# Kernel tuning notes

Measured on AMD Instinct MI355X. Metric: run time of the kernel, lower is better.

Reference implementation:

```python
import jax, jax.numpy as jnp
import numpy as np

N_NODES = 50000
N_EDGES = 800000
IN_SIZE = 128
HIDDEN = 128   # out_size * 2
OUT_SIZE = 64


def setup_inputs() -> dict:
    key = jax.random.key(0)
    ks = jax.random.split(key, 6)
    h = jax.random.normal(ks[0], (N_NODES, IN_SIZE), dtype=jnp.float32)
    W1 = jax.random.normal(ks[1], (IN_SIZE, HIDDEN), dtype=jnp.float32) * (1.0 / np.sqrt(IN_SIZE))
    b1 = jnp.zeros((HIDDEN,), dtype=jnp.float32)
    W2 = jax.random.normal(ks[2], (HIDDEN, OUT_SIZE), dtype=jnp.float32) * (1.0 / np.sqrt(HIDDEN))
    b2 = jnp.zeros((OUT_SIZE,), dtype=jnp.float32)
    src = jax.random.randint(ks[3], (N_EDGES,), 0, N_NODES, dtype=jnp.int64)
    dst = jax.random.randint(ks[4], (N_EDGES,), 0, N_NODES, dtype=jnp.int64)
    return {"h": h, "W1": W1, "b1": b1, "W2": W2, "b2": b2, "src": src, "dst": dst}


def _norms(src, dst, n_nodes):
    # DGL GraphConv norm='both': scale by out_degree^{-1/2} (src side)
    # and in_degree^{-1/2} (dst side); zero degrees clamped to 1.
    ones = jnp.ones(src.shape, dtype=jnp.float32)
    out_deg = jnp.maximum(jax.ops.segment_sum(ones, src, num_segments=n_nodes), 1.0)
    in_deg = jnp.maximum(jax.ops.segment_sum(ones, dst, num_segments=n_nodes), 1.0)
    return (out_deg ** -0.5)[:, None], (in_deg ** -0.5)[:, None]


def _graph_conv(x, W, b, src, dst, norm_out, norm_in, n_nodes):
    # h' = D_in^{-1/2} A D_out^{-1/2} x W + b
    x = x * norm_out                                   # [N, F]
    agg = jax.ops.segment_sum(x[src], dst, num_segments=n_nodes)  # SpMM: [N, F]
    return (agg * norm_in) @ W + b


def reference(h, W1, b1, W2, b2, src, dst):
    n_nodes = h.shape[0]
    norm_out, norm_in = _norms(src, dst, n_nodes)
    h = jax.nn.relu(_graph_conv(h, W1, b1, src, dst, norm_out, norm_in, n_nodes))
    h = jax.nn.relu(_graph_conv(h, W2, b2, src, dst, norm_out, norm_in, n_nodes))
    return h
```

## Files before the change

### kernel.cpp

```cpp
#include <hip/hip_runtime.h>

#define N_NODES 50000
#define N_EDGES 800000
#define CHUNKS 128
#define CHUNK_EDGES 6250
#define NBS 196
#define GA_BLOCKS 391
#define PLACE_BLOCKS 3125

typedef __attribute__((ext_vector_type(8))) short bf16x8;
typedef __attribute__((ext_vector_type(4))) float f32x4;

static __device__ inline unsigned short bf16_rne(float x) {
    unsigned ua = __float_as_uint(x);
    return (unsigned short)((ua + 0x7fffu + ((ua >> 16) & 1u)) >> 16);
}

static __device__ inline unsigned short f16_bits(float x) {
    _Float16 hx = (_Float16)x;
    return __builtin_bit_cast(unsigned short, hx);
}

static __device__ inline float f16_val(unsigned short u) {
    return (float)__builtin_bit_cast(_Float16, u);
}

static __device__ inline float2 unpack_f16x2(unsigned u) {
    _Float16 lo = __builtin_bit_cast(_Float16, (unsigned short)(u & 0xffffu));
    _Float16 hi = __builtin_bit_cast(_Float16, (unsigned short)(u >> 16));
    return make_float2((float)lo, (float)hi);
}

__global__ __launch_bounds__(1024) void hist_wpack_kernel(const int* __restrict__ src,
                                                          const int* __restrict__ dst,
                                                          unsigned char* __restrict__ cntD,
                                                          unsigned char* __restrict__ cntS,
                                                          unsigned char* __restrict__ rp,
                                                          const float* __restrict__ W1,
                                                          const float* __restrict__ W2,
                                                          unsigned short* __restrict__ wf_hi,
                                                          unsigned short* __restrict__ wf_lo,
                                                          unsigned short* __restrict__ wf2_hi,
                                                          unsigned short* __restrict__ wf2_lo) {
    const int t = threadIdx.x;
    const int b = blockIdx.x;

    if (b >= 2 * CHUNKS) {
        int idx = (b - 2 * CHUNKS) * 1024 + t;
        if (idx < 2048) {
            int l  = idx & 63;
            int ct = (idx >> 6) & 7;
            int ks = idx >> 9;
            int col = ct * 16 + (l & 15);
            int k0  = ks * 32 + (l >> 4) * 8;
            unsigned short hi[8], lo[8];
            #pragma unroll
            for (int j = 0; j < 8; ++j) {
                float x = W1[(size_t)(k0 + j) * 128 + col];
                unsigned short h16 = bf16_rne(x);
                hi[j] = h16;
                lo[j] = bf16_rne(x - __uint_as_float((unsigned)h16 << 16));
            }
            ((uint4*)wf_hi)[idx] = *(const uint4*)hi;
            ((uint4*)wf_lo)[idx] = *(const uint4*)lo;
        } else if (idx < 3072) {
            int i2 = idx - 2048;
            int l  = i2 & 63;
            int ct = (i2 >> 6) & 3;
            int ks = i2 >> 8;
            int col = ct * 16 + (l & 15);
            int k0  = ks * 32 + (l >> 4) * 8;
            unsigned short hi[8], lo[8];
            #pragma unroll
            for (int j = 0; j < 8; ++j) {
                float x = W2[(size_t)(k0 + j) * 64 + col];
                unsigned short h16 = bf16_rne(x);
                hi[j] = h16;
                lo[j] = bf16_rne(x - __uint_as_float((unsigned)h16 << 16));
            }
            ((uint4*)wf2_hi)[i2] = *(const uint4*)hi;
            ((uint4*)wf2_lo)[i2] = *(const uint4*)lo;
        }
        return;
    }

    const int c    = b >> 1;
    const int half = b & 1;
    const int nbase = half * 25000;

    __shared__ unsigned hD[6250];
    __shared__ unsigned hS[6250];
    for (int i = t; i < 6250; i += 1024) { hD[i] = 0u; hS[i] = 0u; }
    __syncthreads();

    const int base = c * CHUNK_EDGES;
    for (int i = t; i < CHUNK_EDGES; i += 1024) {
        int e = base + i;
        int d = dst[e];
        int s = src[e];
        unsigned dn = (unsigned)(d - nbase);
        if (dn < 25000u) {
            unsigned shd = (dn & 3u) * 8u;
            unsigned old = atomicAdd(&hD[dn >> 2], 1u << shd);
            rp[e] = (unsigned char)((old >> shd) & 0xffu);
        }
        unsigned sn = (unsigned)(s - nbase);
        if (sn < 25000u)
            atomicAdd(&hS[sn >> 2], 1u << ((sn & 3u) * 8u));
    }
    __syncthreads();

    unsigned* gD = (unsigned*)cntD + (size_t)c * 12500 + half * 6250;
    unsigned* gS = (unsigned*)cntS + (size_t)c * 12500 + half * 6250;
    for (int i = t; i < 6250; i += 1024) { gD[i] = hD[i]; gS[i] = hS[i]; }
}

__global__ __launch_bounds__(256) void deg_scan_kernel(unsigned char* __restrict__ cntD,
                                                       const unsigned char* __restrict__ cntS,
                                                       int* __restrict__ row_ptr,
                                                       int* __restrict__ bsum,
                                                       float* __restrict__ norm_out,
                                                       float* __restrict__ norm_in) {
    const int t = threadIdx.x, lane = t & 63, w = t >> 6;
    const int n = blockIdx.x * 256 + t;
    unsigned sumD = 0u, sumS = 0u;
    if (n < N_NODES) {
        #pragma unroll 4
        for (int c = 0; c < CHUNKS; ++c) {
            size_t idx = (size_t)c * 50000 + n;
            unsigned v = cntD[idx];
            cntD[idx] = (unsigned char)sumD;
            sumD += v;
            sumS += cntS[idx];
        }
        norm_in[n]  = rsqrtf((float)(sumD ? sumD : 1u));
        norm_out[n] = rsqrtf((float)(sumS ? sumS : 1u));
    }
    __shared__ int wsum[4];
    int v = (n < N_NODES) ? (int)sumD : 0;
    int incl = v;
    #pragma unroll
    for (int d = 1; d < 64; d <<= 1) {
        int u = __shfl_up(incl, d, 64);
        if (lane >= d) incl += u;
    }
    if (lane == 63) wsum[w] = incl;
    __syncthreads();
    int woff = 0, total = 0;
    #pragma unroll
    for (int j = 0; j < 4; ++j) {
        int s = wsum[j];
        if (j < w) woff += s;
        total += s;
    }
    if (n < N_NODES) row_ptr[n] = woff + incl - v;
    if (t == 0) bsum[blockIdx.x] = total;
}

__global__ __launch_bounds__(64) void scan2_kernel(int* __restrict__ bsum,
                                                   int* __restrict__ row_ptr) {
    const int lane = threadIdx.x;
    int carry = 0;
    for (int base = 0; base < NBS; base += 64) {
        int t = base + lane;
        int v = (t < NBS) ? bsum[t] : 0;
        int incl = v;
        #pragma unroll
        for (int d = 1; d < 64; d <<= 1) {
            int u = __shfl_up(incl, d, 64);
            if (lane >= d) incl += u;
        }
        int excl = carry + incl - v;
        if (t < NBS) bsum[t] = excl;
        if (t == NBS - 1) row_ptr[N_NODES] = N_EDGES - excl;
        carry += __shfl(incl, 63, 64);
    }
}

__global__ __launch_bounds__(256) void gemmA_place_kernel(const float* __restrict__ h,
                                                          const unsigned short* __restrict__ wf_hi,
                                                          const unsigned short* __restrict__ wf_lo,
                                                          const float* __restrict__ norm_out,
                                                          unsigned short* __restrict__ t1,
                                                          const int* __restrict__ src,
                                                          const int* __restrict__ dst,
                                                          const int* __restrict__ row_ptr,
                                                          const int* __restrict__ bsum,
                                                          const unsigned char* __restrict__ cntD,
                                                          const unsigned char* __restrict__ rp,
                                                          int* __restrict__ eidx) {
    if (blockIdx.x >= GA_BLOCKS) {
        int e = (blockIdx.x - GA_BLOCKS) * 256 + threadIdx.x;
        if (e < N_EDGES) {
            int d = dst[e];
            int c = e / CHUNK_EDGES;
            int pos = row_ptr[d] + bsum[d >> 8] + (int)cntD[(size_t)c * 50000 + d]
                    + (int)rp[e];
            eidx[pos] = src[e];
        }
        return;
    }

    const int t  = threadIdx.x;
    const int wv = t >> 6;
    const int l  = t & 63;
    const int lrow = l & 15;
    const int g    = l >> 4;
    const int n0 = blockIdx.x * 128 + wv * 32;

    int r0 = n0 + lrow;      if (r0 > N_NODES - 1) r0 = N_NODES - 1;
    int r1 = n0 + 16 + lrow; if (r1 > N_NODES - 1) r1 = N_NODES - 1;
    const float* h0 = h + (size_t)r0 * 128 + g * 8;
    const float* h1 = h + (size_t)r1 * 128 + g * 8;

    f32x4 acc[2][8];
    #pragma unroll
    for (int rt = 0; rt < 2; ++rt)
        #pragma unroll
        for (int ct = 0; ct < 8; ++ct)
            acc[rt][ct] = (f32x4){0.f, 0.f, 0.f, 0.f};

    const bf16x8* bh_base = (const bf16x8*)wf_hi;
    const bf16x8* bl_base = (const bf16x8*)wf_lo;

    for (int ks = 0; ks < 4; ++ks) {
        float a0[8], a1[8];
        *(float4*)(a0)     = *(const float4*)(h0 + ks * 32);
        *(float4*)(a0 + 4) = *(const float4*)(h0 + ks * 32 + 4);
        *(float4*)(a1)     = *(const float4*)(h1 + ks * 32);
        *(float4*)(a1 + 4) = *(const float4*)(h1 + ks * 32 + 4);

        bf16x8 a0h, a0l, a1h, a1l;
        #pragma unroll
        for (int j = 0; j < 8; ++j) {
            unsigned short hh = bf16_rne(a0[j]);
            a0h[j] = (short)hh;
            a0l[j] = (short)bf16_rne(a0[j] - __uint_as_float((unsigned)hh << 16));
            unsigned short h2 = bf16_rne(a1[j]);
            a1h[j] = (short)h2;
            a1l[j] = (short)bf16_rne(a1[j] - __uint_as_float((unsigned)h2 << 16));
        }

        #pragma unroll
        for (int ct = 0; ct < 8; ++ct) {
            const int fi = (ks * 8 + ct) * 64 + l;
            bf16x8 bh = bh_base[fi];
            bf16x8 bl = bl_base[fi];
            acc[0][ct] = __builtin_amdgcn_mfma_f32_16x16x32_bf16(a0l, bh, acc[0][ct], 0, 0, 0);
            acc[0][ct] = __builtin_amdgcn_mfma_f32_16x16x32_bf16(a0h, bl, acc[0][ct], 0, 0, 0);
            acc[0][ct] = __builtin_amdgcn_mfma_f32_16x16x32_bf16(a0h, bh, acc[0][ct], 0, 0, 0);
            acc[1][ct] = __builtin_amdgcn_mfma_f32_16x16x32_bf16(a1l, bh, acc[1][ct], 0, 0, 0);
            acc[1][ct] = __builtin_amdgcn_mfma_f32_16x16x32_bf16(a1h, bl, acc[1][ct], 0, 0, 0);
            acc[1][ct] = __builtin_amdgcn_mfma_f32_16x16x32_bf16(a1h, bh, acc[1][ct], 0, 0, 0);
        }
    }

    #pragma unroll
    for (int rt = 0; rt < 2; ++rt) {
        float no_[4];
        #pragma unroll
        for (int r = 0; r < 4; ++r) {
            int row = n0 + rt * 16 + g * 4 + r;
            no_[r] = (row < N_NODES) ? norm_out[row] : 0.f;
        }
        #pragma unroll
        for (int ct = 0; ct < 8; ++ct) {
            #pragma unroll
            for (int r = 0; r < 4; ++r) {
                int row = n0 + rt * 16 + g * 4 + r;
                if (row < N_NODES)
                    t1[(size_t)row * 128 + ct * 16 + lrow] = bf16_rne(acc[rt][ct][r] * no_[r]);
            }
        }
    }
}

__global__ __launch_bounds__(256) void gemmB_kernel(const unsigned short* __restrict__ h1p16,
                                                    const unsigned short* __restrict__ wf2_hi,
                                                    const unsigned short* __restrict__ wf2_lo,
                                                    unsigned short* __restrict__ t2h) {
    const int t  = threadIdx.x;
    const int wv = t >> 6;
    const int l  = t & 63;
    const int lrow = l & 15;
    const int g    = l >> 4;
    const int n0 = blockIdx.x * 128 + wv * 32;

    int r0 = n0 + lrow;      if (r0 > N_NODES - 1) r0 = N_NODES - 1;
    int r1 = n0 + 16 + lrow; if (r1 > N_NODES - 1) r1 = N_NODES - 1;
    const unsigned short* h0 = h1p16 + (size_t)r0 * 128 + g * 8;
    const unsigned short* h1 = h1p16 + (size_t)r1 * 128 + g * 8;

    f32x4 acc[2][4];
    #pragma unroll
    for (int rt = 0; rt < 2; ++rt)
        #pragma unroll
        for (int ct = 0; ct < 4; ++ct)
            acc[rt][ct] = (f32x4){0.f, 0.f, 0.f, 0.f};

    const bf16x8* bh_base = (const bf16x8*)wf2_hi;
    const bf16x8* bl_base = (const bf16x8*)wf2_lo;

    for (int ks = 0; ks < 4; ++ks) {
        unsigned short a0u[8], a1u[8];
        *(uint4*)a0u = *(const uint4*)(h0 + ks * 32);
        *(uint4*)a1u = *(const uint4*)(h1 + ks * 32);

        bf16x8 a0h, a0l, a1h, a1l;
        #pragma unroll
        for (int j = 0; j < 8; ++j) {
            float x0 = f16_val(a0u[j]);
            unsigned short hh = bf16_rne(x0);
            a0h[j] = (short)hh;
            a0l[j] = (short)bf16_rne(x0 - __uint_as_float((unsigned)hh << 16));
            float x1 = f16_val(a1u[j]);
            unsigned short h2 = bf16_rne(x1);
            a1h[j] = (short)h2;
            a1l[j] = (short)bf16_rne(x1 - __uint_as_float((unsigned)h2 << 16));
        }

        #pragma unroll
        for (int ct = 0; ct < 4; ++ct) {
            const int fi = (ks * 4 + ct) * 64 + l;
            bf16x8 bh = bh_base[fi];
            bf16x8 bl = bl_base[fi];
            acc[0][ct] = __builtin_amdgcn_mfma_f32_16x16x32_bf16(a0l, bh, acc[0][ct], 0, 0, 0);
            acc[0][ct] = __builtin_amdgcn_mfma_f32_16x16x32_bf16(a0h, bl, acc[0][ct], 0, 0, 0);
            acc[0][ct] = __builtin_amdgcn_mfma_f32_16x16x32_bf16(a0h, bh, acc[0][ct], 0, 0, 0);
            acc[1][ct] = __builtin_amdgcn_mfma_f32_16x16x32_bf16(a1l, bh, acc[1][ct], 0, 0, 0);
            acc[1][ct] = __builtin_amdgcn_mfma_f32_16x16x32_bf16(a1h, bl, acc[1][ct], 0, 0, 0);
            acc[1][ct] = __builtin_amdgcn_mfma_f32_16x16x32_bf16(a1h, bh, acc[1][ct], 0, 0, 0);
        }
    }

    #pragma unroll
    for (int rt = 0; rt < 2; ++rt) {
        #pragma unroll
        for (int ct = 0; ct < 4; ++ct) {
            #pragma unroll
            for (int r = 0; r < 4; ++r) {
                int row = n0 + rt * 16 + g * 4 + r;
                if (row < N_NODES)
                    t2h[(size_t)row * 64 + ct * 16 + lrow] = f16_bits(acc[rt][ct][r]);
            }
        }
    }
}

__global__ __launch_bounds__(256) void pull128_kernel(const unsigned short* __restrict__ xb,
                                                      const int* __restrict__ row_ptr,
                                                      const int* __restrict__ bsum,
                                                      const int* __restrict__ eidx,
                                                      const float* __restrict__ b1,
                                                      const float* __restrict__ norm_in,
                                                      const float* __restrict__ norm_out,
                                                      unsigned* __restrict__ out16) {
    int node = blockIdx.x * 4 + (threadIdx.x >> 6);
    node = __builtin_amdgcn_readfirstlane(node);
    const int lane = threadIdx.x & 63;
    const int beg = __builtin_amdgcn_readfirstlane(row_ptr[node] + bsum[node >> 8]);
    const int end = __builtin_amdgcn_readfirstlane(row_ptr[node + 1] + bsum[(node + 1) >> 8]);

    float2 acc0 = make_float2(0.f, 0.f);
    float2 acc1 = make_float2(0.f, 0.f);
    float2 acc2 = make_float2(0.f, 0.f);
    float2 acc3 = make_float2(0.f, 0.f);

    for (int base = beg; base < end; base += 64) {
        const int cnt = min(64, end - base);
        int my_e = (lane < cnt) ? eidx[base + lane] : 0;
        int k = 0;
        for (; k + 7 < cnt; k += 8) {
            int s0 = __builtin_amdgcn_readlane(my_e, k);
            int s1 = __builtin_amdgcn_readlane(my_e, k + 1);
            int s2 = __builtin_amdgcn_readlane(my_e, k + 2);
            int s3 = __builtin_amdgcn_readlane(my_e, k + 3);
            int s4 = __builtin_amdgcn_readlane(my_e, k + 4);
            int s5 = __builtin_amdgcn_readlane(my_e, k + 5);
            int s6 = __builtin_amdgcn_readlane(my_e, k + 6);
            int s7 = __builtin_amdgcn_readlane(my_e, k + 7);
            unsigned u0 = ((const unsigned*)(xb + (size_t)s0 * 128))[lane];
            unsigned u1 = ((const unsigned*)(xb + (size_t)s1 * 128))[lane];
            unsigned u2 = ((const unsigned*)(xb + (size_t)s2 * 128))[lane];
            unsigned u3 = ((const unsigned*)(xb + (size_t)s3 * 128))[lane];
            unsigned u4 = ((const unsigned*)(xb + (size_t)s4 * 128))[lane];
            unsigned u5 = ((const unsigned*)(xb + (size_t)s5 * 128))[lane];
            unsigned u6 = ((const unsigned*)(xb + (size_t)s6 * 128))[lane];
            unsigned u7 = ((const unsigned*)(xb + (size_t)s7 * 128))[lane];
            acc0.x += __uint_as_float(u0 << 16);
            acc0.y += __uint_as_float(u0 & 0xffff0000u);
            acc1.x += __uint_as_float(u1 << 16);
            acc1.y += __uint_as_float(u1 & 0xffff0000u);
            acc2.x += __uint_as_float(u2 << 16);
            acc2.y += __uint_as_float(u2 & 0xffff0000u);
            acc3.x += __uint_as_float(u3 << 16);
            acc3.y += __uint_as_float(u3 & 0xffff0000u);
            acc0.x += __uint_as_float(u4 << 16);
            acc0.y += __uint_as_float(u4 & 0xffff0000u);
            acc1.x += __uint_as_float(u5 << 16);
            acc1.y += __uint_as_float(u5 & 0xffff0000u);
            acc2.x += __uint_as_float(u6 << 16);
            acc2.y += __uint_as_float(u6 & 0xffff0000u);
            acc3.x += __uint_as_float(u7 << 16);
            acc3.y += __uint_as_float(u7 & 0xffff0000u);
        }
        for (; k + 3 < cnt; k += 4) {
            int s0 = __builtin_amdgcn_readlane(my_e, k);
            int s1 = __builtin_amdgcn_readlane(my_e, k + 1);
            int s2 = __builtin_amdgcn_readlane(my_e, k + 2);
            int s3 = __builtin_amdgcn_readlane(my_e, k + 3);
            unsigned u0 = ((const unsigned*)(xb + (size_t)s0 * 128))[lane];
            unsigned u1 = ((const unsigned*)(xb + (size_t)s1 * 128))[lane];
            unsigned u2 = ((const unsigned*)(xb + (size_t)s2 * 128))[lane];
            unsigned u3 = ((const unsigned*)(xb + (size_t)s3 * 128))[lane];
            acc0.x += __uint_as_float(u0 << 16);
            acc0.y += __uint_as_float(u0 & 0xffff0000u);
            acc1.x += __uint_as_float(u1 << 16);
            acc1.y += __uint_as_float(u1 & 0xffff0000u);
            acc2.x += __uint_as_float(u2 << 16);
            acc2.y += __uint_as_float(u2 & 0xffff0000u);
            acc3.x += __uint_as_float(u3 << 16);
            acc3.y += __uint_as_float(u3 & 0xffff0000u);
        }
        for (; k < cnt; ++k) {
            int s0 = __builtin_amdgcn_readlane(my_e, k);
            unsigned u0 = ((const unsigned*)(xb + (size_t)s0 * 128))[lane];
            acc0.x += __uint_as_float(u0 << 16);
            acc0.y += __uint_as_float(u0 & 0xffff0000u);
        }
    }

    float ni = norm_in[node];
    float no = norm_out[node];
    float2 bb = ((const float2*)b1)[lane];
    float sx = (acc0.x + acc1.x) + (acc2.x + acc3.x);
    float sy = (acc0.y + acc1.y) + (acc2.y + acc3.y);
    float rx = fmaxf(fmaf(sx, ni, bb.x), 0.f) * no;
    float ry = fmaxf(fmaf(sy, ni, bb.y), 0.f) * no;
    unsigned pw = (unsigned)f16_bits(rx) | ((unsigned)f16_bits(ry) << 16);
    out16[(size_t)node * 64 + lane] = pw;
}

__global__ __launch_bounds__(256) void pull64_kernel(const unsigned* __restrict__ x,
                                                     const int* __restrict__ row_ptr,
                                                     const int* __restrict__ bsum,
                                                     const int* __restrict__ eidx,
                                                     const float* __restrict__ b2,
                                                     const float* __restrict__ norm_in,
                                                     float* __restrict__ out) {
    int node = blockIdx.x * 4 + (threadIdx.x >> 6);
    node = __builtin_amdgcn_readfirstlane(node);
    const int lane = threadIdx.x & 63;
    const int half = lane >> 5;
    const int fl = lane & 31;
    const int beg = __builtin_amdgcn_readfirstlane(row_ptr[node] + bsum[node >> 8]);
    const int end = __builtin_amdgcn_readfirstlane(row_ptr[node + 1] + bsum[(node + 1) >> 8]);

    float2 a0 = make_float2(0.f, 0.f);
    float2 a1 = make_float2(0.f, 0.f);
    float2 a2 = make_float2(0.f, 0.f);
    float2 a3 = make_float2(0.f, 0.f);

    for (int base = beg; base < end; base += 64) {
        const int cnt = min(64, end - base);
        int my_e = (lane < cnt) ? eidx[base + lane] : 0;
        int k = 0;
        for (; k + 7 < cnt; k += 8) {
            int sa0 = __builtin_amdgcn_readlane(my_e, k);
            int sb0 = __builtin_amdgcn_readlane(my_e, k + 1);
            int sa1 = __builtin_amdgcn_readlane(my_e, k + 2);
            int sb1 = __builtin_amdgcn_readlane(my_e, k + 3);
            int sa2 = __builtin_amdgcn_readlane(my_e, k + 4);
            int sb2 = __builtin_amdgcn_readlane(my_e, k + 5);
            int sa3 = __builtin_amdgcn_readlane(my_e, k + 6);
            int sb3 = __builtin_amdgcn_readlane(my_e, k + 7);
            int e0 = half ? sb0 : sa0;
            int e1 = half ? sb1 : sa1;
            int e2 = half ? sb2 : sa2;
            int e3 = half ? sb3 : sa3;
            unsigned u0 = x[(size_t)e0 * 32 + fl];
            unsigned u1 = x[(size_t)e1 * 32 + fl];
            unsigned u2 = x[(size_t)e2 * 32 + fl];
            unsigned u3 = x[(size_t)e3 * 32 + fl];
            float2 v0 = unpack_f16x2(u0);
            float2 v1 = unpack_f16x2(u1);
            float2 v2 = unpack_f16x2(u2);
            float2 v3 = unpack_f16x2(u3);
            a0.x += v0.x; a0.y += v0.y;
            a1.x += v1.x; a1.y += v1.y;
            a2.x += v2.x; a2.y += v2.y;
            a3.x += v3.x; a3.y += v3.y;
        }
        for (; k + 1 < cnt; k += 2) {
            int sa = __builtin_amdgcn_readlane(my_e, k);
            int sb = __builtin_amdgcn_readlane(my_e, k + 1);
            int e0 = half ? sb : sa;
            unsigned u = x[(size_t)e0 * 32 + fl];
            float2 v = unpack_f16x2(u);
            a0.x += v.x; a0.y += v.y;
        }
        if (k < cnt) {
            int sa = __builtin_amdgcn_readlane(my_e, k);
            if (half == 0) {
                unsigned u = x[(size_t)sa * 32 + fl];
                float2 v = unpack_f16x2(u);
                a0.x += v.x; a0.y += v.y;
            }
        }
    }

    float ax = (a0.x + a1.x) + (a2.x + a3.x);
    float ay = (a0.y + a1.y) + (a2.y + a3.y);
    ax += __shfl_xor(ax, 32, 64);
    ay += __shfl_xor(ay, 32, 64);
    if (half == 0) {
        float ni = norm_in[node];
        float2 bb = ((const float2*)b2)[fl];
        float2 r;
        r.x = fmaxf(fmaf(ax, ni, bb.x), 0.f);
        r.y = fmaxf(fmaf(ay, ni, bb.y), 0.f);
        ((float2*)(out + (size_t)node * 64))[fl] = r;
    }
}

extern "C" void kernel_launch(void* const* d_in, const int* in_sizes, int n_in,
                              void* d_out, int out_size, void* d_ws, size_t ws_size,
                              hipStream_t stream) {
    const float* h  = (const float*)d_in[0];
    const float* W1 = (const float*)d_in[1];
    const float* b1 = (const float*)d_in[2];
    const float* W2 = (const float*)d_in[3];
    const float* b2 = (const float*)d_in[4];
    const int* src  = (const int*)d_in[5];
    const int* dst  = (const int*)d_in[6];
    float* out = (float*)d_out;

    char* ws = (char*)d_ws;
    size_t off = 0;
    auto alloc = [&](size_t bytes) {
        void* p = ws + off;
        off = (off + bytes + 255) & ~(size_t)255;
        return p;
    };
    float* norm_out   = (float*)alloc(N_NODES * sizeof(float));
    float* norm_in    = (float*)alloc(N_NODES * sizeof(float));
    int* row_ptr      = (int*)alloc((N_NODES + 1) * sizeof(int));
    int* bsum         = (int*)alloc(NBS * sizeof(int));
    unsigned short* wf_hi  = (unsigned short*)alloc(2048 * 16);
    unsigned short* wf_lo  = (unsigned short*)alloc(2048 * 16);
    unsigned short* wf2_hi = (unsigned short*)alloc(1024 * 16);
    unsigned short* wf2_lo = (unsigned short*)alloc(1024 * 16);
    int* eidx         = (int*)alloc((size_t)N_EDGES * sizeof(int));
    unsigned short* t1 = (unsigned short*)alloc((size_t)N_NODES * 128 * sizeof(short));
    unsigned char* scratch = (unsigned char*)alloc(26 * 1024 * 1024);

    unsigned char* cntD = scratch;
    unsigned char* cntS = cntD + (size_t)CHUNKS * 50000;
    unsigned char* rp   = cntS + (size_t)CHUNKS * 50000;
    unsigned short* h1p16 = (unsigned short*)scratch;
    unsigned short* t2h = t1;

    hist_wpack_kernel<<<2 * CHUNKS + 3, 1024, 0, stream>>>(src, dst, cntD, cntS, rp,
                                                           W1, W2, wf_hi, wf_lo,
                                                           wf2_hi, wf2_lo);

    deg_scan_kernel<<<NBS, 256, 0, stream>>>(cntD, cntS, row_ptr, bsum, norm_out, norm_in);

    scan2_kernel<<<1, 64, 0, stream>>>(bsum, row_ptr);

    gemmA_place_kernel<<<GA_BLOCKS + PLACE_BLOCKS, 256, 0, stream>>>(
        h, wf_hi, wf_lo, norm_out, t1, src, dst, row_ptr, bsum, cntD, rp, eidx);

    pull128_kernel<<<N_NODES / 4, 256, 0, stream>>>(t1, row_ptr, bsum, eidx, b1,
                                                    norm_in, norm_out, (unsigned*)h1p16);

    gemmB_kernel<<<GA_BLOCKS, 256, 0, stream>>>(h1p16, wf2_hi, wf2_lo, t2h);

    pull64_kernel<<<N_NODES / 4, 256, 0, stream>>>((const unsigned*)t2h, row_ptr, bsum, eidx,
                                                   b2, norm_in, out);
}
```

Baseline: 201.7 us.

## Split feature dimension into 64-byte slabs and run gather passes per slab

```diff
diff --git a/kernel.cpp b/kernel.cpp
--- a/kernel.cpp
+++ b/kernel.cpp
@@ -7,6 +7,7 @@
 #define NBS 196
 #define GA_BLOCKS 391
 #define PLACE_BLOCKS 3125
+#define PULL_BLOCKS 12500
 
 typedef __attribute__((ext_vector_type(8))) short bf16x8;
 typedef __attribute__((ext_vector_type(4))) float f32x4;
@@ -29,6 +30,10 @@
     _Float16 lo = __builtin_bit_cast(_Float16, (unsigned short)(u & 0xffffu));
     _Float16 hi = __builtin_bit_cast(_Float16, (unsigned short)(u >> 16));
     return make_float2((float)lo, (float)hi);
+}
+
+static __device__ inline int bperm_i(int idx, int v) {
+    return __builtin_amdgcn_ds_bpermute(idx << 2, v);
 }
 
 __global__ __launch_bounds__(1024) void hist_wpack_kernel(const int* __restrict__ src,
@@ -269,9 +274,83 @@
             for (int r = 0; r < 4; ++r) {
                 int row = n0 + rt * 16 + g * 4 + r;
                 if (row < N_NODES)
-                    t1[(size_t)row * 128 + ct * 16 + lrow] = bf16_rne(acc[rt][ct][r] * no_[r]);
+                    t1[((size_t)(ct >> 1) * N_NODES + row) * 32 + (ct & 1) * 16 + lrow]
+                        = bf16_rne(acc[rt][ct][r] * no_[r]);
             }
         }
+    }
+}
+
+__global__ __launch_bounds__(256) void pull128q_kernel(const unsigned* __restrict__ t1u,
+                                                       const int* __restrict__ row_ptr,
+                                                       const int* __restrict__ bsum,
+                                                       const int* __restrict__ eidx,
+                                                       const float* __restrict__ b1,
+                                                       const float* __restrict__ norm_in,
+                                                       const float* __restrict__ norm_out,
+                                                       unsigned* __restrict__ h1p16,
+                                                       int q) {
+    int node = blockIdx.x * 4 + (threadIdx.x >> 6);
+    node = __builtin_amdgcn_readfirstlane(node);
+    const int lane = threadIdx.x & 63;
+    const int g4 = lane >> 4;
+    const int fl = lane & 15;
+    const int beg = __builtin_amdgcn_readfirstlane(row_ptr[node] + bsum[node >> 8]);
+    const int end = __builtin_amdgcn_readfirstlane(row_ptr[node + 1] + bsum[(node + 1) >> 8]);
+
+    const unsigned* xq = t1u + (size_t)q * N_NODES * 16;
+
+    float2 a0 = make_float2(0.f, 0.f);
+    float2 a1 = make_float2(0.f, 0.f);
+
+    for (int base = beg; base < end; base += 64) {
+        const int cnt = min(64, end - base);
+        const int cm1 = cnt - 1;
+        int my_e = (lane < cnt) ? eidx[base + lane] : 0;
+        int k = 0;
+        for (; k + 16 <= cnt; k += 16) {
+            int s0 = bperm_i(k + g4, my_e);
+            int s1 = bperm_i(k + 4 + g4, my_e);
+            int s2 = bperm_i(k + 8 + g4, my_e);
+            int s3 = bperm_i(k + 12 + g4, my_e);
+            unsigned u0 = xq[(size_t)s0 * 16 + fl];
+            unsigned u1 = xq[(size_t)s1 * 16 + fl];
+            unsigned u2 = xq[(size_t)s2 * 16 + fl];
+            unsigned u3 = xq[(size_t)s3 * 16 + fl];
+            a0.x += __uint_as_float(u0 << 16);
+            a0.y += __uint_as_float(u0 & 0xffff0000u);
+            a1.x += __uint_as_float(u1 << 16);
+            a1.y += __uint_as_float(u1 & 0xffff0000u);
+            a0.x += __uint_as_float(u2 << 16);
+            a0.y += __uint_as_float(u2 & 0xffff0000u);
+            a1.x += __uint_as_float(u3 << 16);
+            a1.y += __uint_as_float(u3 & 0xffff0000u);
+        }
+        for (; k < cnt; k += 4) {
+            int ir = k + g4;
+            int s0 = bperm_i(min(ir, cm1), my_e);
+            unsigned u0 = xq[(size_t)s0 * 16 + fl];
+            if (ir > cm1) u0 = 0u;
+            a0.x += __uint_as_float(u0 << 16);
+            a0.y += __uint_as_float(u0 & 0xffff0000u);
+        }
+    }
+
+    float sx = a0.x + a1.x;
+    float sy = a0.y + a1.y;
+    sx += __shfl_xor(sx, 16, 64);
+    sy += __shfl_xor(sy, 16, 64);
+    sx += __shfl_xor(sx, 32, 64);
+    sy += __shfl_xor(sy, 32, 64);
+
+    if (g4 == 0) {
+        float ni = norm_in[node];
+        float no = norm_out[node];
+        float2 bb = ((const float2*)b1)[q * 16 + fl];
+        float rx = fmaxf(fmaf(sx, ni, bb.x), 0.f) * no;
+        float ry = fmaxf(fmaf(sy, ni, bb.y), 0.f) * no;
+        unsigned pw = (unsigned)f16_bits(rx) | ((unsigned)f16_bits(ry) << 16);
+        h1p16[((size_t)q * N_NODES + node) * 16 + fl] = pw;
     }
 }
 
@@ -288,8 +367,6 @@
 
     int r0 = n0 + lrow;      if (r0 > N_NODES - 1) r0 = N_NODES - 1;
     int r1 = n0 + 16 + lrow; if (r1 > N_NODES - 1) r1 = N_NODES - 1;
-    const unsigned short* h0 = h1p16 + (size_t)r0 * 128 + g * 8;
-    const unsigned short* h1 = h1p16 + (size_t)r1 * 128 + g * 8;
 
     f32x4 acc[2][4];
     #pragma unroll
@@ -302,9 +379,11 @@
     const bf16x8* bl_base = (const bf16x8*)wf2_lo;
 
     for (int ks = 0; ks < 4; ++ks) {
+        const unsigned short* h0 = h1p16 + ((size_t)ks * N_NODES + r0) * 32 + g * 8;
+        const unsigned short* h1 = h1p16 + ((size_t)ks * N_NODES + r1) * 32 + g * 8;
         unsigned short a0u[8], a1u[8];
-        *(uint4*)a0u = *(const uint4*)(h0 + ks * 32);
-        *(uint4*)a1u = *(const uint4*)(h1 + ks * 32);
+        *(uint4*)a0u = *(const uint4*)h0;
+        *(uint4*)a1u = *(const uint4*)h1;
 
         bf16x8 a0h, a0l, a1h, a1l;
         #pragma unroll
@@ -341,185 +420,81 @@
             for (int r = 0; r < 4; ++r) {
                 int row = n0 + rt * 16 + g * 4 + r;
                 if (row < N_NODES)
-                    t2h[(size_t)row * 64 + ct * 16 + lrow] = f16_bits(acc[rt][ct][r]);
+                    t2h[((size_t)(ct >> 1) * N_NODES + row) * 32 + (ct & 1) * 16 + lrow]
+                        = f16_bits(acc[rt][ct][r]);
             }
         }
     }
 }
 
-__global__ __launch_bounds__(256) void pull128_kernel(const unsigned short* __restrict__ xb,
+__global__ __launch_bounds__(256) void pull64h_kernel(const unsigned* __restrict__ t2u,
                                                       const int* __restrict__ row_ptr,
                                                       const int* __restrict__ bsum,
                                                       const int* __restrict__ eidx,
-                                                      const float* __restrict__ b1,
+                                                      const float* __restrict__ b2,
                                                       const float* __restrict__ norm_in,
-                                                      const float* __restrict__ norm_out,
-                                                      unsigned* __restrict__ out16) {
+                                                      float* __restrict__ out,
+                                                      int hh) {
     int node = blockIdx.x * 4 + (threadIdx.x >> 6);
     node = __builtin_amdgcn_readfirstlane(node);
     const int lane = threadIdx.x & 63;
+    const int g4 = lane >> 4;
+    const int fl = lane & 15;
     const int beg = __builtin_amdgcn_readfirstlane(row_ptr[node] + bsum[node >> 8]);
     const int end = __builtin_amdgcn_readfirstlane(row_ptr[node + 1] + bsum[(node + 1) >> 8]);
 
-    float2 acc0 = make_float2(0.f, 0.f);
-    float2 acc1 = make_float2(0.f, 0.f);
-    float2 acc2 = make_float2(0.f, 0.f);
-    float2 acc3 = make_float2(0.f, 0.f);
+    const unsigned* xh = t2u + (size_t)hh * N_NODES * 16;
+
+    float2 a0 = make_float2(0.f, 0.f);
+    float2 a1 = make_float2(0.f, 0.f);
 
     for (int base = beg; base < end; base += 64) {
         const int cnt = min(64, end - base);
+        const int cm1 = cnt - 1;
         int my_e = (lane < cnt) ? eidx[base + lane] : 0;
         int k = 0;
-        for (; k + 7 < cnt; k += 8) {
-            int s0 = __builtin_amdgcn_readlane(my_e, k);
-            int s1 = __builtin_amdgcn_readlane(my_e, k + 1);
-            int s2 = __builtin_amdgcn_readlane(my_e, k + 2);
-            int s3 = __builtin_amdgcn_readlane(my_e, k + 3);
-            int s4 = __builtin_amdgcn_readlane(my_e, k + 4);
-            int s5 = __builtin_amdgcn_readlane(my_e, k + 5);
-            int s6 = __builtin_amdgcn_readlane(my_e, k + 6);
-            int s7 = __builtin_amdgcn_readlane(my_e, k + 7);
-            unsigned u0 = ((const unsigned*)(xb + (size_t)s0 * 128))[lane];
-            unsigned u1 = ((const unsigned*)(xb + (size_t)s1 * 128))[lane];
-            unsigned u2 = ((const unsigned*)(xb + (size_t)s2 * 128))[lane];
-            unsigned u3 = ((const unsigned*)(xb + (size_t)s3 * 128))[lane];
-            unsigned u4 = ((const unsigned*)(xb + (size_t)s4 * 128))[lane];
-            unsigned u5 = ((const unsigned*)(xb + (size_t)s5 * 128))[lane];
-            unsigned u6 = ((const unsigned*)(xb + (size_t)s6 * 128))[lane];
-            unsigned u7 = ((const unsigned*)(xb + (size_t)s7 * 128))[lane];
-            acc0.x += __uint_as_float(u0 << 16);
-            acc0.y += __uint_as_float(u0 & 0xffff0000u);
-            acc1.x += __uint_as_float(u1 << 16);
-            acc1.y += __uint_as_float(u1 & 0xffff0000u);
-            acc2.x += __uint_as_float(u2 << 16);
-            acc2.y += __uint_as_float(u2 & 0xffff0000u);
-            acc3.x += __uint_as_float(u3 << 16);
-            acc3.y += __uint_as_float(u3 & 0xffff0000u);
-            acc0.x += __uint_as_float(u4 << 16);
-            acc0.y += __uint_as_float(u4 & 0xffff0000u);
-            acc1.x += __uint_as_float(u5 << 16);
-            acc1.y += __uint_as_float(u5 & 0xffff0000u);
-            acc2.x += __uint_as_float(u6 << 16);
-            acc2.y += __uint_as_float(u6 & 0xffff0000u);
-            acc3.x += __uint_as_float(u7 << 16);
-            acc3.y += __uint_as_float(u7 & 0xffff0000u);
-        }
-        for (; k + 3 < cnt; k += 4) {
-            int s0 = __builtin_amdgcn_readlane(my_e, k);
-            int s1 = __builtin_amdgcn_readlane(my_e, k + 1);
-            int s2 = __builtin_amdgcn_readlane(my_e, k + 2);
-            int s3 = __builtin_amdgcn_readlane(my_e, k + 3);
-            unsigned u0 = ((const unsigned*)(xb + (size_t)s0 * 128))[lane];
-            unsigned u1 = ((const unsigned*)(xb + (size_t)s1 * 128))[lane];
-            unsigned u2 = ((const unsigned*)(xb + (size_t)s2 * 128))[lane];
-            unsigned u3 = ((const unsigned*)(xb + (size_t)s3 * 128))[lane];
-            acc0.x += __uint_as_float(u0 << 16);
-            acc0.y += __uint_as_float(u0 & 0xffff0000u);
-            acc1.x += __uint_as_float(u1 << 16);
-            acc1.y += __uint_as_float(u1 & 0xffff0000u);
-            acc2.x += __uint_as_float(u2 << 16);
-            acc2.y += __uint_as_float(u2 & 0xffff0000u);
-            acc3.x += __uint_as_float(u3 << 16);
-            acc3.y += __uint_as_float(u3 & 0xffff0000u);
-        }
-        for (; k < cnt; ++k) {
-            int s0 = __builtin_amdgcn_readlane(my_e, k);
-            unsigned u0 = ((const unsigned*)(xb + (size_t)s0 * 128))[lane];
-            acc0.x += __uint_as_float(u0 << 16);
-            acc0.y += __uint_as_float(u0 & 0xffff0000u);
-        }
-    }
-
-    float ni = norm_in[node];
-    float no = norm_out[node];
-    float2 bb = ((const float2*)b1)[lane];
-    float sx = (acc0.x + acc1.x) + (acc2.x + acc3.x);
-    float sy = (acc0.y + acc1.y) + (acc2.y + acc3.y);
-    float rx = fmaxf(fmaf(sx, ni, bb.x), 0.f) * no;
-    float ry = fmaxf(fmaf(sy, ni, bb.y), 0.f) * no;
-    unsigned pw = (unsigned)f16_bits(rx) | ((unsigned)f16_bits(ry) << 16);
-    out16[(size_t)node * 64 + lane] = pw;
-}
-
-__global__ __launch_bounds__(256) void pull64_kernel(const unsigned* __restrict__ x,
-                                                     const int* __restrict__ row_ptr,
-                                                     const int* __restrict__ bsum,
-                                                     const int* __restrict__ eidx,
-                                                     const float* __restrict__ b2,
-                                                     const float* __restrict__ norm_in,
-                                                     float* __restrict__ out) {
-    int node = blockIdx.x * 4 + (threadIdx.x >> 6);
-    node = __builtin_amdgcn_readfirstlane(node);
-    const int lane = threadIdx.x & 63;
-    const int half = lane >> 5;
-    const int fl = lane & 31;
-    const int beg = __builtin_amdgcn_readfirstlane(row_ptr[node] + bsum[node >> 8]);
-    const int end = __builtin_amdgcn_readfirstlane(row_ptr[node + 1] + bsum[(node + 1) >> 8]);
-
-    float2 a0 = make_float2(0.f, 0.f);
-    float2 a1 = make_float2(0.f, 0.f);
-    float2 a2 = make_float2(0.f, 0.f);
-    float2 a3 = make_float2(0.f, 0.f);
-
-    for (int base = beg; base < end; base += 64) {
-        const int cnt = min(64, end - base);
-        int my_e = (lane < cnt) ? eidx[base + lane] : 0;
-        int k = 0;
-        for (; k + 7 < cnt; k += 8) {
-            int sa0 = __builtin_amdgcn_readlane(my_e, k);
-            int sb0 = __builtin_amdgcn_readlane(my_e, k + 1);
-            int sa1 = __builtin_amdgcn_readlane(my_e, k + 2);
-            int sb1 = __builtin_amdgcn_readlane(my_e, k + 3);
-            int sa2 = __builtin_amdgcn_readlane(my_e, k + 4);
-            int sb2 = __builtin_amdgcn_readlane(my_e, k + 5);
-            int sa3 = __builtin_amdgcn_readlane(my_e, k + 6);
-            int sb3 = __builtin_amdgcn_readlane(my_e, k + 7);
-            int e0 = half ? sb0 : sa0;
-            int e1 = half ? sb1 : sa1;
-            int e2 = half ? sb2 : sa2;
-            int e3 = half ? sb3 : sa3;
-            unsigned u0 = x[(size_t)e0 * 32 + fl];
-            unsigned u1 = x[(size_t)e1 * 32 + fl];
-            unsigned u2 = x[(size_t)e2 * 32 + fl];
-            unsigned u3 = x[(size_t)e3 * 32 + fl];
+        for (; k + 16 <= cnt; k += 16) {
+            int s0 = bperm_i(k + g4, my_e);
+            int s1 = bperm_i(k + 4 + g4, my_e);
+            int s2 = bperm_i(k + 8 + g4, my_e);
+            int s3 = bperm_i(k + 12 + g4, my_e);
+            unsigned u0 = xh[(size_t)s0 * 16 + fl];
+            unsigned u1 = xh[(size_t)s1 * 16 + fl];
+            unsigned u2 = xh[(size_t)s2 * 16 + fl];
+            unsigned u3 = xh[(size_t)s3 * 16 + fl];
             float2 v0 = unpack_f16x2(u0);
             float2 v1 = unpack_f16x2(u1);
             float2 v2 = unpack_f16x2(u2);
             float2 v3 = unpack_f16x2(u3);
             a0.x += v0.x; a0.y += v0.y;
             a1.x += v1.x; a1.y += v1.y;
-            a2.x += v2.x; a2.y += v2.y;
-            a3.x += v3.x; a3.y += v3.y;
-        }
-        for (; k + 1 < cnt; k += 2) {
-            int sa = __builtin_amdgcn_readlane(my_e, k);
-            int sb = __builtin_amdgcn_readlane(my_e, k + 1);
-            int e0 = half ? sb : sa;
-            unsigned u = x[(size_t)e0 * 32 + fl];
-            float2 v = unpack_f16x2(u);
+            a0.x += v2.x; a0.y += v2.y;
+            a1.x += v3.x; a1.y += v3.y;
+        }
+        for (; k < cnt; k += 4) {
+            int ir = k + g4;
+            int s0 = bperm_i(min(ir, cm1), my_e);
+            unsigned u0 = xh[(size_t)s0 * 16 + fl];
+            if (ir > cm1) u0 = 0u;
+            float2 v = unpack_f16x2(u0);
             a0.x += v.x; a0.y += v.y;
         }
-        if (k < cnt) {
-            int sa = __builtin_amdgcn_readlane(my_e, k);
-            if (half == 0) {
-                unsigned u = x[(size_t)sa * 32 + fl];
-                float2 v = unpack_f16x2(u);
-                a0.x += v.x; a0.y += v.y;
-            }
-        }
-    }
-
-    float ax = (a0.x + a1.x) + (a2.x + a3.x);
-    float ay = (a0.y + a1.y) + (a2.y + a3.y);
-    ax += __shfl_xor(ax, 32, 64);
-    ay += __shfl_xor(ay, 32, 64);
-    if (half == 0) {
+    }
+
+    float sx = a0.x + a1.x;
+    float sy = a0.y + a1.y;
+    sx += __shfl_xor(sx, 16, 64);
+    sy += __shfl_xor(sy, 16, 64);
+    sx += __shfl_xor(sx, 32, 64);
+    sy += __shfl_xor(sy, 32, 64);
+
+    if (g4 == 0) {
         float ni = norm_in[node];
-        float2 bb = ((const float2*)b2)[fl];
+        float2 bb = ((const float2*)b2)[hh * 16 + fl];
         float2 r;
-        r.x = fmaxf(fmaf(ax, ni, bb.x), 0.f);
-        r.y = fmaxf(fmaf(ay, ni, bb.y), 0.f);
-        ((float2*)(out + (size_t)node * 64))[fl] = r;
+        r.x = fmaxf(fmaf(sx, ni, bb.x), 0.f);
+        r.y = fmaxf(fmaf(sy, ni, bb.y), 0.f);
+        ((float2*)(out + (size_t)node * 64 + hh * 32))[fl] = r;
     }
 }
 
@@ -571,11 +546,14 @@
     gemmA_place_kernel<<<GA_BLOCKS + PLACE_BLOCKS, 256, 0, stream>>>(
         h, wf_hi, wf_lo, norm_out, t1, src, dst, row_ptr, bsum, cntD, rp, eidx);
 
-    pull128_kernel<<<N_NODES / 4, 256, 0, stream>>>(t1, row_ptr, bsum, eidx, b1,
-                                                    norm_in, norm_out, (unsigned*)h1p16);
+    for (int q = 0; q < 4; ++q)
+        pull128q_kernel<<<PULL_BLOCKS, 256, 0, stream>>>((const unsigned*)t1, row_ptr, bsum,
+                                                         eidx, b1, norm_in, norm_out,
+                                                         (unsigned*)h1p16, q);
 
     gemmB_kernel<<<GA_BLOCKS, 256, 0, stream>>>(h1p16, wf2_hi, wf2_lo, t2h);
 
-    pull64_kernel<<<N_NODES / 4, 256, 0, stream>>>((const unsigned*)t2h, row_ptr, bsum, eidx,
-                                                   b2, norm_in, out);
-}
+    for (int hh = 0; hh < 2; ++hh)
+        pull64h_kernel<<<PULL_BLOCKS, 256, 0, stream>>>((const unsigned*)t2h, row_ptr, bsum,
+                                                        eidx, b2, norm_in, out, hh);
+}
```

New measurement: 259.8 us. 28.8% more time.
